# Kernel optimization log

Hardware: AMD Instinct MI355X
Metric: run time of the kernel (lower is better)

Reference implementation:

```python
import jax, jax.numpy as jnp
import numpy as np


def _operators_3_to_2(x2d, A, norm):
    # x2d: [b, d, n, n], A: [b, n, n]. Returns the 20 basis tensors, each [b, d, n, n].
    t = lambda a: a.transpose(0, 1, 3, 2)
    shape = x2d.shape
    op1 = jnp.einsum('bdij,bij,bik->bdjk', x2d, A, A) / norm
    op2 = jnp.einsum('bdij,bij,bjk->bdik', x2d, A, A) / norm
    op3 = jnp.einsum('bdij,bik,bjk->bdij', x2d, A, A) / norm
    op4 = jnp.broadcast_to(jnp.einsum('bdij,bij->bdi', x2d, A)[..., None], shape) / norm
    op5 = jnp.broadcast_to(jnp.einsum('bdij,bij->bdj', x2d, A)[..., None], shape) / norm
    op6 = jnp.einsum('bdij,bik->bdjk', x2d, A) / norm
    # NOTE: source has ops7 = [op6, op6.transpose] (bug: op7 computed but unused) -- replicated faithfully.
    op8 = jnp.einsum('bdij,bik->bdij', x2d, A) / norm
    op9 = jnp.einsum('bdij,bjk->bdij', x2d, A) / norm
    op10 = jnp.broadcast_to(x2d.sum(3, keepdims=True), shape) / norm
    op11 = jnp.broadcast_to(x2d.sum(2, keepdims=True), shape) / norm
    return [op1, t(op1), op2, t(op2), op3,
            op4, t(op4), op5, t(op5),
            op6, t(op6), op6, t(op6),
            op8, op9,
            op10, t(op10), op11, t(op11),
            x2d]


def _forward(x, edge_weight, coeffs1, bias1, coeffs2, bias2, edge_index, batch, n):
    f = x.shape[-1]
    b = x.shape[0] // n
    # to_2d_tensor: [b*n, f] -> [b, 2f, n, n]
    x2 = x.reshape(b, n, f).transpose(0, 2, 1)  # [b, f, n]
    x_2d = jnp.concatenate([
        jnp.broadcast_to(x2[:, :, :, None], (b, f, n, n)),
        jnp.broadcast_to(x2[:, :, None, :], (b, f, n, n)),
    ], axis=1)
    # to_dense_adj: scatter-add edge weights into per-graph dense [b, n, n]
    g = batch[edge_index[0]]
    r = edge_index[0] - g * n
    c = edge_index[1] - g * n
    A = jnp.zeros((b, n, n), x.dtype).at[g, r, c].add(edge_weight)
    norm = jnp.asarray(n, x.dtype)  # normalization=True default
    for li, (coeffs, bias) in enumerate([(coeffs1, bias1), (coeffs2, bias2)]):
        ops_out = jnp.stack(_operators_3_to_2(x_2d, A, norm), axis=2)  # [b, d, 20, n, n]
        x_2d = jnp.einsum('der,bdrij->beij', coeffs, ops_out) + bias
        if li == 0:
            x_2d = jax.nn.sigmoid(x_2d)
    return x_2d.mean(axis=(1, 2, 3))  # [b]


def setup_inputs() -> dict:
    key = jax.random.key(0)
    kx, kg, ks, kd, kw, kc1, kc2 = jax.random.split(key, 7)
    b, n, deg, f, h = 4, 128, 16, 32, 32
    d_in, d_out = 2 * f, 2 * h  # layer doubles channels; hidden layer is d_out -> d_out
    E = b * n * deg
    x = jax.random.normal(kx, (b * n, f), dtype=jnp.float32)
    g = jax.random.randint(kg, (E,), 0, b)
    src = jax.random.randint(ks, (E,), 0, n)
    dst = jax.random.randint(kd, (E,), 0, n)
    edge_index = jnp.stack([g * n + src, g * n + dst]).astype(jnp.int32)
    edge_weight = jax.random.uniform(kw, (E,), dtype=jnp.float32)
    batch = (jnp.arange(b * n) // n).astype(jnp.int32)
    scale1 = np.sqrt(2.0) / (d_in + d_out)
    scale2 = np.sqrt(2.0) / (d_out + d_out)
    coeffs1 = jax.random.normal(kc1, (d_in, d_out, 20), dtype=jnp.float32) * scale1
    coeffs2 = jax.random.normal(kc2, (d_out, d_out, 20), dtype=jnp.float32) * scale2
    bias1 = jnp.zeros((1, d_out, 1, 1), dtype=jnp.float32)
    bias2 = jnp.zeros((1, d_out, 1, 1), dtype=jnp.float32)
    return {"x": x, "edge_weight": edge_weight, "coeffs1": coeffs1, "bias1": bias1,
            "coeffs2": coeffs2, "bias2": bias2, "edge_index": edge_index,
            "batch": batch, "n": n}


def reference(x, edge_weight, coeffs1, bias1, coeffs2, bias2, edge_index, batch, n):
    return _forward(x, edge_weight, coeffs1, bias1, coeffs2, bias2, edge_index, batch, n)
```

## Files before the change

### kernel.cpp

```cpp
#include <hip/hip_runtime.h>
#include <stdint.h>

typedef unsigned short u16;
using short8 = __attribute__((ext_vector_type(8))) short;
using f32x4  = __attribute__((ext_vector_type(4))) float;

#define NB 4
#define NN 128
#define NF 32
#define ND 64
#define NMAT (NB*ND*NN*NN)

#define OFF_A     0u
#define OFF_ACC   262144u
#define OFF_AAT   262400u
#define OFF_RA    524544u
#define OFF_W     526592u
#define OFF_RM    1116416u
#define OFF_CM    1247488u
#define OFF_RX    1378560u
#define OFF_CX    1509632u
#define OFF_BF    1640960u
#define OFF_ATB   1641472u
#define OFF_WB    1772544u
#define OFF_X2    1936384u
#define OFF_XC    10324992u
#define OFF_CA    10357760u
#define OFF_UA    18713600u
#define OFF_UB    27102208u
#define OFF_UC    35490816u
#define OFF_UD    43879424u
#define OFF_YACC  52268032u

__device__ __forceinline__ float b2f(u16 v){
  union { uint32_t u; float f; } x; x.u = ((uint32_t)v) << 16; return x.f;
}
__device__ __forceinline__ u16 f2b(float f){
  union { uint32_t u; float f2; } x; x.f2 = f;
  uint32_t u = x.u;
  return (u16)((u + 0x7FFFu + ((u >> 16) & 1u)) >> 16);
}

#define MFMA16(a,b,c) __builtin_amdgcn_mfma_f32_16x16x32_bf16((a),(b),(c),0,0,0)

__device__ __constant__ signed char dR1[18] = {0,9,1,10,2,3,4,13,14,19,5,7,15,18,6,8,16,17};
__device__ __constant__ signed char dR2[18] = {-1,11,-1,12,-1,-1,-1,-1,-1,-1,-1,-1,-1,-1,-1,-1,-1,-1};

__global__ void k_setup(const int* __restrict__ ei, const int* __restrict__ bat,
                        const void* __restrict__ ews, float* __restrict__ A, int E,
                        const void* __restrict__ xs, u16* __restrict__ xc,
                        const void* __restrict__ c1s, const void* __restrict__ c2s,
                        const void* __restrict__ b1s, const void* __restrict__ b2s,
                        float* __restrict__ W, u16* __restrict__ Wb,
                        float* __restrict__ bfv)
{
  __shared__ int flg;
  const u16* x16 = (const u16*)xs;
  if (threadIdx.x == 0) flg = 0;
  __syncthreads();
  int hit = 0;
  for (int k = threadIdx.x; k < 1024; k += 256){
    u16 u = x16[k];
    if (((u >> 7) & 0xFF) >= 0x90) hit = 1;
  }
  if (hit) flg = 1;
  __syncthreads();
  const int isf = flg;

  const int bx = blockIdx.x;
  if (bx < 32){
    if (bx == 0 && threadIdx.x < 128){
      int tt = threadIdx.x;
      const void* bsrc = (tt < 64) ? b1s : b2s;
      int idx = tt & 63;
      bfv[tt] = isf ? ((const float*)bsrc)[idx] : b2f(((const u16*)bsrc)[idx]);
    }
    for (int t = bx*256 + threadIdx.x; t < E; t += 32*256){
      int s = ei[t], dnode = ei[E + t];
      int g = bat[s];
      int r = s - g*NN, c = dnode - g*NN;
      float wv = isf ? ((const float*)ews)[t] : b2f(((const u16*)ews)[t]);
      atomicAdd(&A[(g*NN + r)*NN + c], wv);
    }
  } else if (bx < 40){
    int idx8 = ((bx - 32)*256 + threadIdx.x)*8;
    if (!isf){
      *(short8*)(xc + idx8) = *(const short8*)(x16 + idx8);
    } else {
      const float* xfp = (const float*)xs;
      short8 v;
      #pragma unroll
      for (int k = 0; k < 8; k++) v[k] = (short)f2b(xfp[idx8 + k]);
      *(short8*)(xc + idx8) = v;
    }
  } else {
    int gl = (bx - 40)*256 + threadIdx.x;
    if (gl >= 2*1152*64) return;
    int L = gl / (1152*64);
    int rem = gl - L*1152*64;
    int row = rem >> 6, e = rem & 63;
    int slot = row >> 6, d = row & 63;
    const void* cr = L ? c2s : c1s;
    int base = (d*64 + e)*20;
    int i1 = base + dR1[slot];
    float v = isf ? ((const float*)cr)[i1] : b2f(((const u16*)cr)[i1]);
    if (dR2[slot] >= 0){
      int i2 = base + dR2[slot];
      v += isf ? ((const float*)cr)[i2] : b2f(((const u16*)cr)[i2]);
    }
    float scale = (slot == 9) ? 1.0f : (1.0f/128.0f);
    v *= scale;
    W[gl] = v;
    if (slot < 10)
      Wb[(((size_t)L*10 + slot)*64 + e)*64 + d] = f2b(v);
  }
}

__global__ __launch_bounds__(256) void k_prepA(const float* __restrict__ A, float* __restrict__ AAt,
                                               u16* __restrict__ ATb, float* __restrict__ rA,
                                               float* __restrict__ cA){
  const int iq = blockIdx.x, b = blockIdx.y;
  const int t = threadIdx.x;
  if (iq < 32){
    int j = t & 127, ih = t >> 7;
    int i0 = iq*4 + ih, i1 = i0 + 2;
    const float* Ab = A + b*NN*NN;
    float acc0 = 0.f, acc1 = 0.f;
    #pragma unroll 4
    for (int k = 0; k < 128; k += 4){
      float4 aj = *(const float4*)(Ab + j*128 + k);
      float4 a0 = *(const float4*)(Ab + i0*128 + k);
      float4 a1 = *(const float4*)(Ab + i1*128 + k);
      acc0 += a0.x*aj.x + a0.y*aj.y + a0.z*aj.z + a0.w*aj.w;
      acc1 += a1.x*aj.x + a1.y*aj.y + a1.z*aj.z + a1.w*aj.w;
    }
    AAt[(b*NN + i0)*NN + j] = acc0;
    AAt[(b*NN + i1)*NN + j] = acc1;
  } else {
    __shared__ float lds[128][129];
    for (int l = 0; l < 64; l++){
      int idx = l*256 + t;
      lds[idx >> 7][idx & 127] = A[b*16384 + idx];
    }
    __syncthreads();
    for (int l = 0; l < 64; l++){
      int idx = l*256 + t;
      int r = idx >> 7, c = idx & 127;
      ATb[b*16384 + idx] = f2b(lds[c][r]);
    }
    if (t < 128){
      float s = 0.f;
      for (int j = 0; j < 128; j++) s += lds[t][j];
      rA[b*NN + t] = s;
    } else {
      int c = t - 128;
      float s = 0.f;
      for (int j = 0; j < 128; j++) s += lds[j][c];
      cA[b*NN + c] = s;
    }
  }
}

#define SJ32 70
#define SJF  67
#define SXE  34

__global__ __launch_bounds__(256) void k_mixrow(const u16* __restrict__ Xs, const float* __restrict__ A,
    const float* __restrict__ AAt, const float* __restrict__ rA, const float* __restrict__ cA,
    const u16* __restrict__ xc, const u16* __restrict__ Wb,
    u16* __restrict__ Ua, u16* __restrict__ Ub, u16* __restrict__ Uc, u16* __restrict__ Ud,
    float* __restrict__ Yacc,
    float* __restrict__ RM, float* __restrict__ CM,
    float* __restrict__ RX, float* __restrict__ CXv, int first)
{
  const int b = blockIdx.y;
  const int t = threadIdx.x;

  if (blockIdx.x >= 256){
    const int d = blockIdx.x - 256;
    if (first){
      if (t < 128){
        const int i = t;
        if (d < NF){
          float xv = b2f(xc[(b*NN + i)*NF + d]);
          RM[(b*64 + d)*128 + i] = xv * rA[b*NN + i];
          RX[(b*64 + d)*128 + i] = 128.f * xv;
        } else {
          const u16* xcb = xc + b*NN*NF + (d - NF);
          const float* Ar = A + b*16384 + i*128;
          float sm = 0.f, sx = 0.f;
          for (int j = 0; j < 128; j++){
            float xj = b2f(xcb[j*NF]);
            sm += Ar[j]*xj; sx += xj;
          }
          RM[(b*64 + d)*128 + i] = sm;
          RX[(b*64 + d)*128 + i] = sx;
        }
      } else {
        const int j = t - 128;
        if (d < NF){
          const u16* xcb = xc + b*NN*NF + d;
          const float* Ac = A + b*16384 + j;
          float sm = 0.f, sx = 0.f;
          for (int i = 0; i < 128; i++){
            float xi = b2f(xcb[i*NF]);
            sm += Ac[i*128]*xi; sx += xi;
          }
          CM[(b*64 + d)*128 + j] = sm;
          CXv[(b*64 + d)*128 + j] = sx;
        } else {
          float xv = b2f(xc[(b*NN + j)*NF + (d - NF)]);
          CM[(b*64 + d)*128 + j] = xv * cA[b*NN + j];
          CXv[(b*64 + d)*128 + j] = 128.f * xv;
        }
      }
      return;
    }
    const u16* Xd = Xs + ((size_t)(b*ND + d) << 14);
    const float* Ab = A + b*NN*NN;
    float sm = 0.f, sx = 0.f;
    if (t < 128){
      const int i = t;
      #pragma unroll 2
      for (int j8 = 0; j8 < 16; j8++){
        short8 xv = *(const short8*)(Xd + i*128 + j8*8);
        float4 a0 = *(const float4*)(Ab + i*128 + j8*8);
        float4 a1 = *(const float4*)(Ab + i*128 + j8*8 + 4);
        float x0 = b2f((u16)xv[0]), x1 = b2f((u16)xv[1]), x2 = b2f((u16)xv[2]), x3 = b2f((u16)xv[3]);
        float x4 = b2f((u16)xv[4]), x5 = b2f((u16)xv[5]), x6 = b2f((u16)xv[6]), x7 = b2f((u16)xv[7]);
        sx += x0+x1+x2+x3+x4+x5+x6+x7;
        sm += x0*a0.x + x1*a0.y + x2*a0.z + x3*a0.w
            + x4*a1.x + x5*a1.y + x6*a1.z + x7*a1.w;
      }
      RM[(b*64 + d)*128 + i] = sm;
      RX[(b*64 + d)*128 + i] = sx;
    } else {
      const int j = t - 128;
      for (int i = 0; i < 128; i++){
        float xv = b2f(Xd[i*128 + j]);
        sx += xv;
        sm += xv * Ab[i*128 + j];
      }
      CM[(b*64 + d)*128 + j] = sm;
      CXv[(b*64 + d)*128 + j] = sx;
    }
    return;
  }

  const int w = t >> 6, lane = t & 63;
  const int col = lane & 15, quad = lane >> 4;
  const int ij0 = blockIdx.x*64;

  __shared__ uint32_t lsb[4][32*SJ32];
  __shared__ float lsf[64*SJF];

  short8 wa[10][2];
  #pragma unroll
  for (int s = 0; s < 10; s++){
    const u16* wp = Wb + (size_t)((s*64 + w*16 + col)*64 + quad*8);
    wa[s][0] = *(const short8*)wp;
    wa[s][1] = *(const short8*)(wp + 32);
  }
  float a_s[4], t_s[4], rjv[4];
  #pragma unroll
  for (int sj = 0; sj < 4; sj++){
    int ij = ij0 + sj*16 + col;
    a_s[sj] = A[b*16384 + ij];
    t_s[sj] = AAt[b*16384 + ij];
    rjv[sj] = rA[b*128 + (ij & 127)];
  }
  const float riv = rA[b*128 + (ij0 >> 7)];

  uint32_t* ldsX = &lsb[0][0];
  {
    const int ep = t >> 3;
    const int s8 = (t & 7)*8;
    if (first){
      const int i = ij0 >> 7;
      const int j0 = (ij0 & 127) + s8;
      if (ep < 16){
        uint32_t p = *(const uint32_t*)(xc + (b*NN + i)*NF + 2*ep);
        #pragma unroll
        for (int k = 0; k < 8; k++) ldsX[(s8 + k)*SXE + ep] = p;
      } else {
        const int d0 = 2*ep - 32;
        #pragma unroll
        for (int k = 0; k < 8; k++)
          ldsX[(s8 + k)*SXE + ep] = *(const uint32_t*)(xc + (b*NN + j0 + k)*NF + d0);
      }
    } else {
      const u16* xp = Xs + ((size_t)(b*ND + 2*ep) << 14) + ij0 + s8;
      short8 r0 = *(const short8*)xp;
      short8 r1 = *(const short8*)(xp + 16384);
      #pragma unroll
      for (int k = 0; k < 8; k++)
        ldsX[(s8 + k)*SXE + ep] = ((uint32_t)(u16)r0[k]) | (((uint32_t)(u16)r1[k]) << 16);
    }
  }
  __syncthreads();
  short8 xb[4][2];
  #pragma unroll
  for (int sj = 0; sj < 4; sj++){
    #pragma unroll
    for (int h = 0; h < 2; h++){
      const uint32_t* p = &ldsX[(sj*16 + col)*SXE + quad*4 + h*16];
      uint2 u0 = *(const uint2*)p;
      uint2 u1 = *(const uint2*)(p + 2);
      union { uint32_t u[4]; short8 s; } cv;
      cv.u[0] = u0.x; cv.u[1] = u0.y; cv.u[2] = u1.x; cv.u[3] = u1.y;
      xb[sj][h] = cv.s;
    }
  }
  __syncthreads();

  #pragma unroll
  for (int g = 0; g < 5; g++){
    const int s0_tab[5]  = {0, 2, 4, 5, 6};
    const int nsl_tab[5] = {2, 2, 1, 1, 4};
    const int s0 = s0_tab[g], nsl = nsl_tab[g];
    #pragma unroll
    for (int sj = 0; sj < 4; sj++){
      f32x4 acc[4];
      #pragma unroll
      for (int s = 0; s < 4; s++) acc[s] = (f32x4){0.f,0.f,0.f,0.f};
      #pragma unroll
      for (int s = 0; s < 4; s++){
        if (s >= nsl) break;
        acc[s] = MFMA16(wa[s0+s][0], xb[sj][0], acc[s]);
        acc[s] = MFMA16(wa[s0+s][1], xb[sj][1], acc[s]);
      }
      if (g < 4){
        float v[4];
        #pragma unroll
        for (int r = 0; r < 4; r++){
          if (g == 2 || g == 3) v[r] = acc[0][r]*a_s[sj];
          else                  v[r] = acc[0][r]*a_s[sj] + acc[1][r];
        }
        uint32_t p0 = (uint32_t)f2b(v[0]) | ((uint32_t)f2b(v[1]) << 16);
        uint32_t p1 = (uint32_t)f2b(v[2]) | ((uint32_t)f2b(v[3]) << 16);
        int ep = w*8 + quad*2;
        lsb[g][ep*SJ32 + sj*16 + col] = p0;
        lsb[g][(ep + 1)*SJ32 + sj*16 + col] = p1;
      } else {
        #pragma unroll
        for (int r = 0; r < 4; r++){
          float v = acc[0][r]*t_s[sj] + acc[1][r]*riv + acc[2][r]*rjv[sj] + acc[3][r];
          lsf[(w*16 + quad*4 + r)*SJF + sj*16 + col] = v;
        }
      }
    }
  }
  __syncthreads();

  const int eo = t >> 2, seg = t & 3;
  const int ep = eo >> 1, sh = (eo & 1)*16;
  #pragma unroll
  for (int g = 0; g < 4; g++){
    const uint32_t* lp = &lsb[g][ep*SJ32 + seg*16];
    short8 v0, v1;
    #pragma unroll
    for (int k = 0; k < 8; k++){
      v0[k] = (short)((lp[k]   >> sh) & 0xffffu);
      v1[k] = (short)((lp[8+k] >> sh) & 0xffffu);
    }
    u16* U = (g==0)?Ua:(g==1)?Ub:(g==2)?Uc:Ud;
    u16* dst = U + ((size_t)(b*64 + eo) << 14) + ij0 + seg*16;
    *(short8*)dst = v0;
    *(short8*)(dst + 8) = v1;
  }
  {
    const float* fp = &lsf[eo*SJF + seg*16];
    float* dst = Yacc + ((size_t)(b*64 + eo) << 14) + ij0 + seg*16;
    #pragma unroll
    for (int q = 0; q < 4; q++)
      *(float4*)(dst + q*4) = make_float4(fp[q*4], fp[q*4+1], fp[q*4+2], fp[q*4+3]);
  }
}

#define SLT 68

__global__ __launch_bounds__(256) void k_tne(const u16* __restrict__ ATb,
    const u16* __restrict__ Ua, const u16* __restrict__ Ub,
    const u16* __restrict__ Uc, const u16* __restrict__ Ud,
    const float* __restrict__ Yacc, const float* __restrict__ W,
    const float* __restrict__ RM, const float* __restrict__ CM,
    const float* __restrict__ RX, const float* __restrict__ CXv,
    const float* __restrict__ bias, u16* __restrict__ Xout, float* __restrict__ acc4, int last)
{
  const int nh = blockIdx.x, be = blockIdx.y;
  const int b = be >> 6, e = be & 63;
  const int t = threadIdx.x, wave = t >> 6, lane = t & 63;
  const int col = lane & 15, quad = lane >> 4;
  const int m0 = (wave >> 1)*64;
  const int n0 = nh*64 + (wave & 1)*32;
  const int nb0 = nh*64;

  __shared__ uint32_t uls[128*SLT];
  __shared__ uint32_t ubl[64*SLT];
  __shared__ float radd[128], cadd[128];
  __shared__ float red[4];

  if (t < 128){
    int i = t; float s = 0.f;
    for (int d = 0; d < ND; d++){
      int v = (b*ND + d)*NN + i;
      s += W[(640 + d)*64 + e]*RM[v] + W[(704 + d)*64 + e]*CM[v]
         + W[(768 + d)*64 + e]*RX[v] + W[(832 + d)*64 + e]*CXv[v];
    }
    radd[i] = s;
  } else {
    int j = t - 128; float s = 0.f;
    for (int d = 0; d < ND; d++){
      int v = (b*ND + d)*NN + j;
      s += W[(896 + d)*64 + e]*RM[v] + W[(960 + d)*64 + e]*CM[v]
         + W[(1024 + d)*64 + e]*RX[v] + W[(1088 + d)*64 + e]*CXv[v];
    }
    cadd[j] = s;
  }

  const u16* ua = Ua + ((size_t)be << 14);
  const u16* ub = Ub + ((size_t)be << 14);
  {
    const int kp = t >> 2;
    #pragma unroll
    for (int it = 0; it < 4; it++){
      int mo = it*4 + (t & 3);
      short8 r0 = *(const short8*)(ua + (2*kp)*128 + mo*8);
      short8 r1 = *(const short8*)(ua + (2*kp + 1)*128 + mo*8);
      #pragma unroll
      for (int x = 0; x < 8; x++)
        uls[(mo*8 + x)*SLT + kp] = ((uint32_t)(u16)r0[x]) | (((uint32_t)(u16)r1[x]) << 16);
    }
    #pragma unroll
    for (int it = 0; it < 2; it++){
      int no = it*4 + (t & 3);
      short8 r0 = *(const short8*)(ub + (2*kp)*128 + nb0 + no*8);
      short8 r1 = *(const short8*)(ub + (2*kp + 1)*128 + nb0 + no*8);
      #pragma unroll
      for (int x = 0; x < 8; x++)
        ubl[(no*8 + x)*SLT + kp] = ((uint32_t)(u16)r0[x]) | (((uint32_t)(u16)r1[x]) << 16);
    }
  }
  __syncthreads();

  f32x4 acc[4][2];
  #pragma unroll
  for (int mt = 0; mt < 4; mt++)
    #pragma unroll
    for (int nt = 0; nt < 2; nt++)
      acc[mt][nt] = (f32x4){0.f,0.f,0.f,0.f};

  const u16* at = ATb + ((size_t)b << 14);
  short8 at_n[4][2];
  #pragma unroll
  for (int kq = 0; kq < 4; kq++){
    int k0 = kq*32 + quad*8;
    at_n[kq][0] = *(const short8*)(at + (n0 + col)*128 + k0);
    at_n[kq][1] = *(const short8*)(at + (n0 + 16 + col)*128 + k0);
  }

  #pragma unroll
  for (int kq = 0; kq < 4; kq++){
    int kd = kq*16 + quad*4;
    #pragma unroll
    for (int mt = 0; mt < 4; mt++){
      short8 af = *(const short8*)&uls[(m0 + mt*16 + col)*SLT + kd];
      acc[mt][0] = MFMA16(af, at_n[kq][0], acc[mt][0]);
      acc[mt][1] = MFMA16(af, at_n[kq][1], acc[mt][1]);
    }
  }
  #pragma unroll
  for (int kq = 0; kq < 4; kq++){
    int k0 = kq*32 + quad*8, kd = kq*16 + quad*4;
    short8 bf0 = *(const short8*)&ubl[((wave & 1)*32 + 0*16 + col)*SLT + kd];
    short8 bf1 = *(const short8*)&ubl[((wave & 1)*32 + 1*16 + col)*SLT + kd];
    #pragma unroll
    for (int mt = 0; mt < 4; mt++){
      short8 af = *(const short8*)(at + (m0 + mt*16 + col)*128 + k0);
      acc[mt][0] = MFMA16(af, bf0, acc[mt][0]);
      acc[mt][1] = MFMA16(af, bf1, acc[mt][1]);
    }
  }
  {
    const u16* uc = Uc + ((size_t)be << 14);
    #pragma unroll
    for (int kq = 0; kq < 4; kq++){
      int k0 = kq*32 + quad*8;
      #pragma unroll
      for (int mt = 0; mt < 4; mt++){
        short8 af = *(const short8*)(uc + (m0 + mt*16 + col)*128 + k0);
        acc[mt][0] = MFMA16(af, at_n[kq][0], acc[mt][0]);
        acc[mt][1] = MFMA16(af, at_n[kq][1], acc[mt][1]);
      }
    }
  }
  {
    const u16* ud = Ud + ((size_t)be << 14);
    #pragma unroll
    for (int kq = 0; kq < 4; kq++){
      int k0 = kq*32 + quad*8;
      short8 bf0 = *(const short8*)(ud + (n0 + col)*128 + k0);
      short8 bf1 = *(const short8*)(ud + (n0 + 16 + col)*128 + k0);
      #pragma unroll
      for (int mt = 0; mt < 4; mt++){
        short8 af = *(const short8*)(at + (m0 + mt*16 + col)*128 + k0);
        acc[mt][0] = MFMA16(af, bf0, acc[mt][0]);
        acc[mt][1] = MFMA16(af, bf1, acc[mt][1]);
      }
    }
  }
  __syncthreads();

  uint32_t* stg = uls;
  const float bv = bias[e];
  const float* Y = Yacc + ((size_t)be << 14);
  if (!last){
    #pragma unroll
    for (int mt = 0; mt < 4; mt++)
      #pragma unroll
      for (int nt = 0; nt < 2; nt++)
        #pragma unroll
        for (int rp = 0; rp < 2; rp++){
          uint32_t p = 0;
          #pragma unroll
          for (int h = 0; h < 2; h++){
            int r = rp*2 + h;
            int row = m0 + mt*16 + quad*4 + r;
            int cn = n0 + nt*16 + col;
            float v = acc[mt][nt][r] + Y[row*128 + cn] + radd[row] + cadd[cn] + bv;
            v = 1.f/(1.f + __expf(-v));
            p |= ((uint32_t)f2b(v)) << (16*h);
          }
          int ipair = (m0 + mt*16 + quad*4) >> 1;
          stg[(ipair + rp)*SLT + (wave & 1)*32 + nt*16 + col] = p;
        }
    __syncthreads();
    const uint32_t* lp = &stg[(t >> 2)*SLT + (t & 1)*32];
    const int sh = ((t >> 1) & 1)*16;
    u16* dst = Xout + ((size_t)be << 14) + (size_t)(t >> 1)*128 + nh*64 + (t & 1)*32;
    #pragma unroll
    for (int q2 = 0; q2 < 4; q2++){
      short8 v;
      #pragma unroll
      for (int k = 0; k < 8; k++) v[k] = (short)((lp[q2*8 + k] >> sh) & 0xffffu);
      *(short8*)(dst + q2*8) = v;
    }
  } else {
    float loc = 0.f;
    #pragma unroll
    for (int mt = 0; mt < 4; mt++)
      #pragma unroll
      for (int nt = 0; nt < 2; nt++)
        #pragma unroll
        for (int r = 0; r < 4; r++){
          int row = m0 + mt*16 + quad*4 + r;
          int cn = n0 + nt*16 + col;
          loc += acc[mt][nt][r] + Y[row*128 + cn] + radd[row] + cadd[cn] + bv;
        }
    for (int off = 32; off > 0; off >>= 1) loc += __shfl_down(loc, off, 64);
    if (lane == 0) red[wave] = loc;
    __syncthreads();
    if (t == 0) atomicAdd(&acc4[b], red[0] + red[1] + red[2] + red[3]);
  }
}

__global__ void k_finish(const float* __restrict__ acc4, const u16* __restrict__ x16,
                         void* __restrict__ out){
  __shared__ int flg;
  int t = threadIdx.x;
  if (t == 0) flg = 0;
  __syncthreads();
  int hit = 0;
  for (int k = t; k < 512; k += 64){
    u16 u = x16[k];
    if (((u >> 7) & 0xFF) >= 0x90) hit = 1;
  }
  if (hit) flg = 1;
  __syncthreads();
  if (t < NB){
    float v = acc4[t] * (1.0f/1048576.0f);
    if (flg) ((float*)out)[t] = v;
    else     ((u16*)out)[t] = f2b(v);
  }
}

extern "C" void kernel_launch(void* const* d_in, const int* in_sizes, int n_in,
                              void* d_out, int out_size, void* d_ws, size_t ws_size,
                              hipStream_t stream)
{
  const void* x   = d_in[0];
  const void* ew  = d_in[1];
  const void* c1  = d_in[2];
  const void* b1  = d_in[3];
  const void* c2  = d_in[4];
  const void* b2  = d_in[5];
  const int* ei  = (const int*)d_in[6];
  const int* bat = (const int*)d_in[7];
  const int E = in_sizes[1];

  char* wsb = (char*)d_ws;
  float* A    = (float*)(wsb + OFF_A);
  float* acc4 = (float*)(wsb + OFF_ACC);
  float* AAt  = (float*)(wsb + OFF_AAT);
  float* rA   = (float*)(wsb + OFF_RA);
  float* W    = (float*)(wsb + OFF_W);
  float* RM   = (float*)(wsb + OFF_RM);
  float* CM   = (float*)(wsb + OFF_CM);
  float* RX   = (float*)(wsb + OFF_RX);
  float* CXv  = (float*)(wsb + OFF_CX);
  float* bfv  = (float*)(wsb + OFF_BF);
  u16* ATb = (u16*)(wsb + OFF_ATB);
  u16* Wb  = (u16*)(wsb + OFF_WB);
  u16* X2  = (u16*)(wsb + OFF_X2);
  u16* xc  = (u16*)(wsb + OFF_XC);
  float* cA = (float*)(wsb + OFF_CA);
  u16* Ua  = (u16*)(wsb + OFF_UA);
  u16* Ub  = (u16*)(wsb + OFF_UB);
  u16* Uc  = (u16*)(wsb + OFF_UC);
  u16* Ud  = (u16*)(wsb + OFF_UD);
  float* Yacc = (float*)(wsb + OFF_YACC);

  hipMemsetAsync(wsb, 0, OFF_AAT, stream);

  k_setup<<<dim3(616), dim3(256), 0, stream>>>(ei, bat, ew, A, E, x, xc,
                                               c1, c2, b1, b2, W, Wb, bfv);
  k_prepA<<<dim3(33, NB), dim3(256), 0, stream>>>(A, AAt, ATb, rA, cA);

  for (int L = 0; L < 2; L++){
    const float* Wl = W + (size_t)L*1152*64;
    const u16*  Wbl = Wb + (size_t)L*10*64*64;
    k_mixrow<<<dim3(320, NB), dim3(256), 0, stream>>>(X2, A, AAt, rA, cA, xc, Wbl,
                                                      Ua, Ub, Uc, Ud, Yacc, RM, CM, RX, CXv,
                                                      L == 0 ? 1 : 0);
    k_tne<<<dim3(2, 256), dim3(256), 0, stream>>>(ATb, Ua, Ub, Uc, Ud, Yacc, Wl,
                                                  RM, CM, RX, CXv, bfv + L*64, X2, acc4, L);
  }
  k_finish<<<dim3(1), dim3(64), 0, stream>>>(acc4, (const u16*)x, d_out);
}
```

Before: 203.8 us.

## Merge k_tne column halves into one 512-thread block and fuse finish kernel

Each (batch, channel) output tile is now handled by a single 512-thread block covering all 128 columns instead of two 256-thread blocks. This removes the duplicated radd/cadd reductions and the repeated Ua staging per half. The final k_finish launch is folded into the last layer's k_tne through an atomic completion counter, so the last block writes the output. That saves one kernel launch but adds a threadfence and atomic per block and halves the grid size.

After: 199.1 us. -2.3%, faster.

```diff
diff --git a/kernel.cpp b/kernel.cpp
--- a/kernel.cpp
+++ b/kernel.cpp
@@ -9,7 +9,6 @@
 #define NN 128
 #define NF 32
 #define ND 64
-#define NMAT (NB*ND*NN*NN)
 
 #define OFF_A     0u
 #define OFF_ACC   262144u
@@ -378,27 +377,35 @@
 }
 
 #define SLT 68
-
-__global__ __launch_bounds__(256) void k_tne(const u16* __restrict__ ATb,
+#define SST 136
+
+__global__ __launch_bounds__(512) void k_tne(const u16* __restrict__ ATb,
     const u16* __restrict__ Ua, const u16* __restrict__ Ub,
     const u16* __restrict__ Uc, const u16* __restrict__ Ud,
     const float* __restrict__ Yacc, const float* __restrict__ W,
     const float* __restrict__ RM, const float* __restrict__ CM,
     const float* __restrict__ RX, const float* __restrict__ CXv,
-    const float* __restrict__ bias, u16* __restrict__ Xout, float* __restrict__ acc4, int last)
+    const float* __restrict__ bias, u16* __restrict__ Xout, float* __restrict__ acc4,
+    unsigned int* __restrict__ cnt, const u16* __restrict__ x16, void* __restrict__ outp,
+    int last)
 {
-  const int nh = blockIdx.x, be = blockIdx.y;
+  const int be = blockIdx.x;
   const int b = be >> 6, e = be & 63;
   const int t = threadIdx.x, wave = t >> 6, lane = t & 63;
   const int col = lane & 15, quad = lane >> 4;
-  const int m0 = (wave >> 1)*64;
-  const int n0 = nh*64 + (wave & 1)*32;
-  const int nb0 = nh*64;
+  const int m0 = (wave >> 2)*64;
+  const int n0 = (wave & 3)*32;
 
   __shared__ uint32_t uls[128*SLT];
-  __shared__ uint32_t ubl[64*SLT];
+  __shared__ uint32_t ubl[128*SLT];
   __shared__ float radd[128], cadd[128];
-  __shared__ float red[4];
+  __shared__ float red[8];
+  __shared__ int flg, lastblk;
+
+  if (t == 0){ flg = 0; lastblk = 0; }
+
+  const u16* ua = Ua + ((size_t)be << 14);
+  const u16* ub = Ub + ((size_t)be << 14);
 
   if (t < 128){
     int i = t; float s = 0.f;
@@ -408,7 +415,7 @@
          + W[(768 + d)*64 + e]*RX[v] + W[(832 + d)*64 + e]*CXv[v];
     }
     radd[i] = s;
-  } else {
+  } else if (t < 256){
     int j = t - 128; float s = 0.f;
     for (int d = 0; d < ND; d++){
       int v = (b*ND + d)*NN + j;
@@ -416,26 +423,26 @@
          + W[(1024 + d)*64 + e]*RX[v] + W[(1088 + d)*64 + e]*CXv[v];
     }
     cadd[j] = s;
-  }
-
-  const u16* ua = Ua + ((size_t)be << 14);
-  const u16* ub = Ub + ((size_t)be << 14);
-  {
-    const int kp = t >> 2;
-    #pragma unroll
-    for (int it = 0; it < 4; it++){
-      int mo = it*4 + (t & 3);
+  } else if (t < 384){
+    const int tt = t - 256;
+    const int kp = tt >> 1, p = tt & 1;
+    #pragma unroll
+    for (int it = 0; it < 8; it++){
+      int mo = it*2 + p;
       short8 r0 = *(const short8*)(ua + (2*kp)*128 + mo*8);
       short8 r1 = *(const short8*)(ua + (2*kp + 1)*128 + mo*8);
       #pragma unroll
       for (int x = 0; x < 8; x++)
         uls[(mo*8 + x)*SLT + kp] = ((uint32_t)(u16)r0[x]) | (((uint32_t)(u16)r1[x]) << 16);
     }
-    #pragma unroll
-    for (int it = 0; it < 2; it++){
-      int no = it*4 + (t & 3);
-      short8 r0 = *(const short8*)(ub + (2*kp)*128 + nb0 + no*8);
-      short8 r1 = *(const short8*)(ub + (2*kp + 1)*128 + nb0 + no*8);
+  } else {
+    const int tt = t - 384;
+    const int kp = tt >> 1, p = tt & 1;
+    #pragma unroll
+    for (int it = 0; it < 8; it++){
+      int no = it*2 + p;
+      short8 r0 = *(const short8*)(ub + (2*kp)*128 + no*8);
+      short8 r1 = *(const short8*)(ub + (2*kp + 1)*128 + no*8);
       #pragma unroll
       for (int x = 0; x < 8; x++)
         ubl[(no*8 + x)*SLT + kp] = ((uint32_t)(u16)r0[x]) | (((uint32_t)(u16)r1[x]) << 16);
@@ -472,8 +479,8 @@
   #pragma unroll
   for (int kq = 0; kq < 4; kq++){
     int k0 = kq*32 + quad*8, kd = kq*16 + quad*4;
-    short8 bf0 = *(const short8*)&ubl[((wave & 1)*32 + 0*16 + col)*SLT + kd];
-    short8 bf1 = *(const short8*)&ubl[((wave & 1)*32 + 1*16 + col)*SLT + kd];
+    short8 bf0 = *(const short8*)&ubl[(n0 + col)*SLT + kd];
+    short8 bf1 = *(const short8*)&ubl[(n0 + 16 + col)*SLT + kd];
     #pragma unroll
     for (int mt = 0; mt < 4; mt++){
       short8 af = *(const short8*)(at + (m0 + mt*16 + col)*128 + k0);
@@ -515,6 +522,7 @@
   const float bv = bias[e];
   const float* Y = Yacc + ((size_t)be << 14);
   if (!last){
+    const int chalf = (n0 >> 6)*68 + (n0 & 32);
     #pragma unroll
     for (int mt = 0; mt < 4; mt++)
       #pragma unroll
@@ -531,13 +539,14 @@
             v = 1.f/(1.f + __expf(-v));
             p |= ((uint32_t)f2b(v)) << (16*h);
           }
-          int ipair = (m0 + mt*16 + quad*4) >> 1;
-          stg[(ipair + rp)*SLT + (wave & 1)*32 + nt*16 + col] = p;
+          int ipair = ((m0 + mt*16 + quad*4) >> 1) + rp;
+          stg[ipair*SST + chalf + nt*16 + col] = p;
         }
     __syncthreads();
-    const uint32_t* lp = &stg[(t >> 2)*SLT + (t & 1)*32];
-    const int sh = ((t >> 1) & 1)*16;
-    u16* dst = Xout + ((size_t)be << 14) + (size_t)(t >> 1)*128 + nh*64 + (t & 1)*32;
+    const int u = t & 255, half = t >> 8;
+    const uint32_t* lp = &stg[(u >> 2)*SST + half*68 + (u & 1)*32];
+    const int sh = ((u >> 1) & 1)*16;
+    u16* dst = Xout + ((size_t)be << 14) + (size_t)(u >> 1)*128 + half*64 + (u & 1)*32;
     #pragma unroll
     for (int q2 = 0; q2 < 4; q2++){
       short8 v;
@@ -560,27 +569,25 @@
     for (int off = 32; off > 0; off >>= 1) loc += __shfl_down(loc, off, 64);
     if (lane == 0) red[wave] = loc;
     __syncthreads();
-    if (t == 0) atomicAdd(&acc4[b], red[0] + red[1] + red[2] + red[3]);
-  }
-}
-
-__global__ void k_finish(const float* __restrict__ acc4, const u16* __restrict__ x16,
-                         void* __restrict__ out){
-  __shared__ int flg;
-  int t = threadIdx.x;
-  if (t == 0) flg = 0;
-  __syncthreads();
-  int hit = 0;
-  for (int k = t; k < 512; k += 64){
-    u16 u = x16[k];
-    if (((u >> 7) & 0xFF) >= 0x90) hit = 1;
-  }
-  if (hit) flg = 1;
-  __syncthreads();
-  if (t < NB){
-    float v = acc4[t] * (1.0f/1048576.0f);
-    if (flg) ((float*)out)[t] = v;
-    else     ((u16*)out)[t] = f2b(v);
+    if (t == 0){
+      float s = 0.f;
+      #pragma unroll
+      for (int wv = 0; wv < 8; wv++) s += red[wv];
+      atomicAdd(&acc4[b], s);
+      __threadfence();
+      unsigned int old = atomicAdd(cnt, 1u);
+      if (old == 255u) lastblk = 1;
+    }
+    __syncthreads();
+    if (lastblk){
+      if (((x16[t] >> 7) & 0xFF) >= 0x90) flg = 1;
+      __syncthreads();
+      if (t < NB){
+        float v = atomicAdd(&acc4[t], 0.f) * (1.0f/1048576.0f);
+        if (flg) ((float*)outp)[t] = v;
+        else     ((u16*)outp)[t] = f2b(v);
+      }
+    }
   }
 }
 
@@ -601,6 +608,7 @@
   char* wsb = (char*)d_ws;
   float* A    = (float*)(wsb + OFF_A);
   float* acc4 = (float*)(wsb + OFF_ACC);
+  unsigned int* cnt = (unsigned int*)(wsb + OFF_ACC + 32);
   float* AAt  = (float*)(wsb + OFF_AAT);
   float* rA   = (float*)(wsb + OFF_RA);
   float* W    = (float*)(wsb + OFF_W);
@@ -632,8 +640,8 @@
     k_mixrow<<<dim3(320, NB), dim3(256), 0, stream>>>(X2, A, AAt, rA, cA, xc, Wbl,
                                                       Ua, Ub, Uc, Ud, Yacc, RM, CM, RX, CXv,
                                                       L == 0 ? 1 : 0);
-    k_tne<<<dim3(2, 256), dim3(256), 0, stream>>>(ATb, Ua, Ub, Uc, Ud, Yacc, Wl,
-                                                  RM, CM, RX, CXv, bfv + L*64, X2, acc4, L);
-  }
-  k_finish<<<dim3(1), dim3(64), 0, stream>>>(acc4, (const u16*)x, d_out);
+    k_tne<<<dim3(256), dim3(512), 0, stream>>>(ATb, Ua, Ub, Uc, Ud, Yacc, Wl,
+                                               RM, CM, RX, CXv, bfv + L*64, X2, acc4,
+                                               cnt, (const u16*)x, d_out, L);
+  }
 }
```
